# Optimization experiments

Hardware: AMD Instinct MI355X
Metric: run time of the kernel (lower is better)

Reference implementation:

```python
import jax, jax.numpy as jnp
import numpy as np
from jax import lax

K = 5        # kernel_size
KN = 32      # kernel_num
C_IN = 16
PRIOR_VAR = 0.01


def _extract_patches(x, k):
    # TF tf.image.extract_patches VALID, stride 1: last-dim order is (kh, kw, c)
    B, H, W, C = x.shape
    Ho, Wo = H - k + 1, W - k + 1
    p = jnp.stack([x[:, i:i + Ho, j:j + Wo, :] for i in range(k) for j in range(k)], axis=3)
    return p.reshape(B, Ho * Wo, k * k * C)  # [B, P, k*k*C]


def setup_inputs() -> dict:
    key = jax.random.key(0)
    k1, k2, k3, k4 = jax.random.split(key, 4)
    mu_in = jax.random.normal(k1, (32, 64, 64, C_IN), dtype=jnp.float32)
    Sigma_in = jax.random.uniform(k2, (32, 64, 64, C_IN), dtype=jnp.float32)
    # GlorotNormal for w_mu
    fan_in = K * K * C_IN
    fan_out = K * K * KN
    std = jnp.sqrt(2.0 / (fan_in + fan_out)).astype(jnp.float32)
    w_mu = jax.random.normal(k3, (K, K, C_IN, KN), dtype=jnp.float32) * std
    w_sigma = jax.random.uniform(k4, (KN,), dtype=jnp.float32, minval=-4.6, maxval=-2.25)
    return {"mu_in": mu_in, "Sigma_in": Sigma_in, "w_mu": w_mu, "w_sigma": w_sigma}


def reference(mu_in, Sigma_in, w_mu, w_sigma):
    B = mu_in.shape[0]
    # KL regularizer (broadcast w_sigma over w_mu shape, mean over all)
    kl_loss = (jnp.log(PRIOR_VAR) - 1.0 - w_sigma
               + jax.nn.softplus(w_sigma) / PRIOR_VAR
               + jnp.square(w_mu) / PRIOR_VAR)
    kl_conv = 0.5 * jnp.mean(kl_loss)

    w_sigma_2 = jax.nn.softplus(w_sigma)  # [KN]

    # mean path: standard conv
    mu_out = lax.conv_general_dilated(
        mu_in, w_mu, window_strides=(1, 1), padding='VALID',
        dimension_numbers=('NHWC', 'HWIO', 'NHWC'))  # [B, Ho, Wo, KN]
    Ho = mu_out.shape[1]

    mu_dim = jnp.float32(K * K * C_IN)

    diag_sigma_g = _extract_patches(Sigma_in, K)          # [B, P, D]
    mu_in_patches = _extract_patches(mu_in, K)            # [B, P, D]

    mu_cov_square = jnp.square(w_mu).reshape(K * K * C_IN, KN)
    mu_wT_sigmags_mu_w = diag_sigma_g @ (mu_cov_square / mu_dim)          # [B, P, KN]
    trace = jnp.sum(diag_sigma_g, axis=2, keepdims=True) * w_sigma_2 / mu_dim  # [B, P, KN]
    mu_gT_mu_g = jnp.sum(jnp.square(mu_in_patches), axis=-1, keepdims=True)    # [B, P, 1]
    sigmaw_mu_gT_mu_g = mu_gT_mu_g * w_sigma_2 / mu_dim                   # [B, P, KN]

    Sigma_out = trace + mu_wT_sigmags_mu_w + sigmaw_mu_gT_mu_g
    Sigma_out = jax.nn.softplus(Sigma_out.reshape(B, Ho, Ho, KN))
    return mu_out, Sigma_out, kl_conv
```

## Files before the change

kernel.cpp:

```cpp
#include <hip/hip_runtime.h>
#include <hip/hip_bf16.h>
#include <math.h>

#define KK 5
#define KN 32
#define CIN 16
#define H 64
#define W 64
#define NB 32
#define HO 60
#define WO 60
#define D_TOT 400
#define OUT_PLANE (NB*HO*WO*KN)

#define TH 8
#define TW 16
#define IN_R 12
#define IN_C 20
#define CPAD 24
#define TILE_SH (IN_R*IN_C*CPAD)
#define NKSTEP 13

typedef short short8 __attribute__((ext_vector_type(8)));
typedef float f32x4 __attribute__((ext_vector_type(4)));

__device__ __forceinline__ ushort f2bf(float x) {
    __hip_bfloat16 h = __float2bfloat16(x);
    return *reinterpret_cast<ushort*>(&h);
}
__device__ __forceinline__ float bf2f(ushort u) {
    __hip_bfloat16 h = *reinterpret_cast<__hip_bfloat16*>(&u);
    return __bfloat162float(h);
}
__device__ __forceinline__ ushort4 pk4(float4 v) {
    union { __hip_bfloat162 h; ushort2 u; } a, b;
    a.h = __float22bfloat162_rn(make_float2(v.x, v.y));
    b.h = __float22bfloat162_rn(make_float2(v.z, v.w));
    ushort4 r;
    r.x = a.u.x; r.y = a.u.y; r.z = b.u.x; r.w = b.u.y;
    return r;
}
__device__ __forceinline__ float softplusf(float x) {
    return (x > 20.0f) ? x : __logf(1.0f + __expf(x));
}

__global__ void prep_all(const float* __restrict__ w_mu, const float* __restrict__ w_sigma,
                         ushort* __restrict__ bmu, ushort* __restrict__ bsq,
                         float* __restrict__ spw, float* __restrict__ kl_out) {
    __shared__ float red[256];
    int t = threadIdx.x;
    if (blockIdx.x < 52) {
        int idx = blockIdx.x * 256 + t;
        int j  = idx & 7;
        int l  = (idx >> 3) & 63;
        int nt = (idx >> 9) & 1;
        int ts = idx >> 10;
        int k  = ts * 32 + ((l >> 4) & 3) * 8 + j;
        int n  = nt * 16 + (l & 15);
        if (k < D_TOT) {
            float w  = w_mu[k * KN + n];
            float sp = log1pf(expf(w_sigma[n]));
            bmu[idx] = f2bf(w);
            bsq[idx] = f2bf((w * w + sp) * (1.0f / 400.0f));
        } else {
            bmu[idx] = 0;
            bsq[idx] = 0;
        }
    } else {
        float s = 0.f;
        for (int i = t; i < D_TOT * KN; i += 256) { float w = w_mu[i]; s += w * w; }
        red[t] = s;
        __syncthreads();
        for (int off = 128; off > 0; off >>= 1) {
            if (t < off) red[t] += red[t + off];
            __syncthreads();
        }
        float sum_w2 = red[0];
        if (t < KN) {
            float ws = w_sigma[t];
            spw[t] = log1pf(expf(ws)) * (1.0f / 400.0f);
        }
        if (t == 0) {
            float sws = 0.f;
            for (int kn = 0; kn < KN; ++kn) {
                float ws = w_sigma[kn];
                float sp = log1pf(expf(ws));
                sws += -ws + sp * 100.0f;
            }
            float kl = 0.5f * (-4.605170186f - 1.0f + sws * (1.0f / 32.0f)
                               + sum_w2 * (100.0f / 12800.0f));
            *kl_out = kl;
        }
    }
}

__global__ __launch_bounds__(256, 4)
void vdp_main(const float* __restrict__ mu_in, const float* __restrict__ sig_in,
              const ushort* __restrict__ bmu_g, const ushort* __restrict__ bsq_g,
              const float* __restrict__ spw,
              float* __restrict__ mu_out, float* __restrict__ sig_out) {
    __shared__ ushort tiles[2 * TILE_SH + 8];
    __shared__ float csum[IN_R * IN_C];
    __shared__ float t12s[TH * TW];

    const int b   = blockIdx.z;
    const int ho0 = blockIdx.y * TH;
    const int wo0 = blockIdx.x * TW;
    const int t   = threadIdx.x;

    if (t < 8) tiles[2 * TILE_SH + t] = 0;

    for (int i = t; i < IN_R * IN_C * 4; i += 256) {
        int row = i / 80;
        int rem = i - row * 80;
        int col = rem >> 2, c4 = rem & 3;
        int gh = ho0 + row, gw = wo0 + col;
        float4 vm = make_float4(0.f, 0.f, 0.f, 0.f), vs = vm;
        if (gh < H && gw < W) {
            size_t g = (((size_t)b * H + gh) * W + gw) * CIN + c4 * 4;
            vm = *(const float4*)(mu_in + g);
            vs = *(const float4*)(sig_in + g);
        }
        int sb = (row * IN_C + col) * CPAD + c4 * 4;
        *(ushort4*)&tiles[sb] = pk4(vm);
        *(ushort4*)&tiles[TILE_SH + sb] = pk4(vs);
    }
    __syncthreads();

    if (t < IN_R * IN_C) {
        int sb = t * CPAD;
        float acc = 0.f;
#pragma unroll
        for (int g = 0; g < 4; ++g) {
            ushort4 m4 = *(ushort4*)&tiles[sb + g * 4];
            float m0 = bf2f(m4.x), m1 = bf2f(m4.y), m2 = bf2f(m4.z), m3 = bf2f(m4.w);
            acc += m0 * m0 + m1 * m1 + m2 * m2 + m3 * m3;
        }
        csum[t] = acc;
    }
    __syncthreads();

    if (t < TH * TW) {
        int r = t >> 4, c = t & 15;
        float s = 0.f;
#pragma unroll
        for (int kh = 0; kh < KK; ++kh)
#pragma unroll
            for (int kw = 0; kw < KK; ++kw)
                s += csum[(r + kh) * IN_C + c + kw];
        t12s[t] = s;
    }
    __syncthreads();

    const int w    = t >> 6;
    const int l    = t & 63;
    const int col  = l & 15;
    const int q    = l >> 4;
    const int qh   = q >> 1;
    const int qc   = q & 1;

    const char* lds = (const char*)tiles;
    int base0 = ((2 * w + 0) * IN_C + col) * (CPAD * 2) + qc * 16;
    int base1 = ((2 * w + 1) * IN_C + col) * (CPAD * 2) + qc * 16;
    const int qh48  = qh * 48;
    const int qh768 = qh * 768;
    const int zpad  = 2 * TILE_SH * 2;
    const int SGOFF = TILE_SH * 2;

    const short8* Bmu8 = (const short8*)bmu_g;
    const short8* Bsq8 = (const short8*)bsq_g;

    f32x4 accm[2][2], accs[2][2];
    f32x4 z = {0.f, 0.f, 0.f, 0.f};
#pragma unroll
    for (int a = 0; a < 2; ++a)
#pragma unroll
        for (int bn = 0; bn < 2; ++bn) { accm[a][bn] = z; accs[a][bn] = z; }

    constexpr int F0v[NKSTEP] = {0, 2, 4, 21, 23, 40, 42, 44, 61, 63, 80, 82, 84};
    constexpr int D16[NKSTEP] = {0, 0, 1, 0, 0, 0, 0, 1, 0, 0, 0, 0, 2};

#pragma unroll
    for (int ts = 0; ts < NKSTEP; ++ts) {
        short8 am0, am1, as0, as1;
        if (D16[ts] == 2) {
            int a0 = qh ? zpad : (base0 + F0v[ts] * 48);
            int a1 = qh ? zpad : (base1 + F0v[ts] * 48);
            am0 = *(const short8*)(lds + a0);
            am1 = *(const short8*)(lds + a1);
            as0 = *(const short8*)(lds + a0 + (qh ? 0 : SGOFF));
            as1 = *(const short8*)(lds + a1 + (qh ? 0 : SGOFF));
        } else {
            int ex = (D16[ts] ? qh768 : qh48) + F0v[ts] * 48;
            am0 = *(const short8*)(lds + base0 + ex);
            am1 = *(const short8*)(lds + base1 + ex);
            as0 = *(const short8*)(lds + SGOFF + base0 + ex);
            as1 = *(const short8*)(lds + SGOFF + base1 + ex);
        }
        short8 bm0 = Bmu8[(ts * 2 + 0) * 64 + l];
        short8 bm1 = Bmu8[(ts * 2 + 1) * 64 + l];
        short8 bs0 = Bsq8[(ts * 2 + 0) * 64 + l];
        short8 bs1 = Bsq8[(ts * 2 + 1) * 64 + l];

        accm[0][0] = __builtin_amdgcn_mfma_f32_16x16x32_bf16(am0, bm0, accm[0][0], 0, 0, 0);
        accm[0][1] = __builtin_amdgcn_mfma_f32_16x16x32_bf16(am0, bm1, accm[0][1], 0, 0, 0);
        accm[1][0] = __builtin_amdgcn_mfma_f32_16x16x32_bf16(am1, bm0, accm[1][0], 0, 0, 0);
        accm[1][1] = __builtin_amdgcn_mfma_f32_16x16x32_bf16(am1, bm1, accm[1][1], 0, 0, 0);
        accs[0][0] = __builtin_amdgcn_mfma_f32_16x16x32_bf16(as0, bs0, accs[0][0], 0, 0, 0);
        accs[0][1] = __builtin_amdgcn_mfma_f32_16x16x32_bf16(as0, bs1, accs[0][1], 0, 0, 0);
        accs[1][0] = __builtin_amdgcn_mfma_f32_16x16x32_bf16(as1, bs0, accs[1][0], 0, 0, 0);
        accs[1][1] = __builtin_amdgcn_mfma_f32_16x16x32_bf16(as1, bs1, accs[1][1], 0, 0, 0);
    }

    const float spw0 = spw[col], spw1 = spw[16 + col];
#pragma unroll
    for (int mt = 0; mt < 2; ++mt) {
        int ho = ho0 + 2 * w + mt;
        if (ho >= HO) continue;
#pragma unroll
        for (int reg = 0; reg < 4; ++reg) {
            int wo = wo0 + q * 4 + reg;
            if (wo >= WO) continue;
            float t12v = t12s[(2 * w + mt) * TW + q * 4 + reg];
            size_t basep = (((size_t)b * HO + ho) * WO + wo) * KN;
            mu_out[basep + col]      = accm[mt][0][reg];
            mu_out[basep + 16 + col] = accm[mt][1][reg];
            float s0 = accs[mt][0][reg] + t12v * spw0;
            float s1 = accs[mt][1][reg] + t12v * spw1;
            sig_out[basep + col]      = softplusf(s0);
            sig_out[basep + 16 + col] = softplusf(s1);
        }
    }
}

extern "C" void kernel_launch(void* const* d_in, const int* in_sizes, int n_in,
                              void* d_out, int out_size, void* d_ws, size_t ws_size,
                              hipStream_t stream) {
    const float* mu_in   = (const float*)d_in[0];
    const float* sig_in  = (const float*)d_in[1];
    const float* w_mu    = (const float*)d_in[2];
    const float* w_sigma = (const float*)d_in[3];

    float* out     = (float*)d_out;
    float* mu_out  = out;
    float* sig_out = out + (size_t)OUT_PLANE;
    float* kl_out  = out + 2 * (size_t)OUT_PLANE;

    ushort* bmu = (ushort*)d_ws;
    ushort* bsq = bmu + 13312;
    float*  spw = (float*)(bsq + 13312);

    prep_all<<<53, 256, 0, stream>>>(w_mu, w_sigma, bmu, bsq, spw, kl_out);
    vdp_main<<<dim3(4, 8, NB), 256, 0, stream>>>(mu_in, sig_in, bmu, bsq, spw,
                                                 mu_out, sig_out);
}
```

Before: 113.0 us.

## Process two batch images per block with register-prefetched double-buffered tiles

Each block now handles two batch images instead of one, halving the grid. The second image's input tile is loaded into registers while the first tile is processed, then written to a second LDS buffer. This aims to hide global load latency behind MFMA work. In exchange it doubles LDS use, lowers the occupancy hint from 4 to 3 blocks, and leaves fewer blocks to fill the GPU.

```diff
diff --git a/kernel.cpp b/kernel.cpp
--- a/kernel.cpp
+++ b/kernel.cpp
@@ -19,7 +19,9 @@
 #define IN_C 20
 #define CPAD 24
 #define TILE_SH (IN_R*IN_C*CPAD)
+#define BUF_BYTES (2*TILE_SH*2)
 #define NKSTEP 13
+#define NLOAD (IN_R*IN_C*4)
 
 typedef short short8 __attribute__((ext_vector_type(8)));
 typedef float f32x4 __attribute__((ext_vector_type(4)));
@@ -94,45 +96,46 @@
     }
 }
 
-__global__ __launch_bounds__(256, 4)
-void vdp_main(const float* __restrict__ mu_in, const float* __restrict__ sig_in,
-              const ushort* __restrict__ bmu_g, const ushort* __restrict__ bsq_g,
-              const float* __restrict__ spw,
-              float* __restrict__ mu_out, float* __restrict__ sig_out) {
-    __shared__ ushort tiles[2 * TILE_SH + 8];
-    __shared__ float csum[IN_R * IN_C];
-    __shared__ float t12s[TH * TW];
-
-    const int b   = blockIdx.z;
-    const int ho0 = blockIdx.y * TH;
-    const int wo0 = blockIdx.x * TW;
-    const int t   = threadIdx.x;
-
-    if (t < 8) tiles[2 * TILE_SH + t] = 0;
-
-    for (int i = t; i < IN_R * IN_C * 4; i += 256) {
-        int row = i / 80;
-        int rem = i - row * 80;
-        int col = rem >> 2, c4 = rem & 3;
-        int gh = ho0 + row, gw = wo0 + col;
-        float4 vm = make_float4(0.f, 0.f, 0.f, 0.f), vs = vm;
-        if (gh < H && gw < W) {
-            size_t g = (((size_t)b * H + gh) * W + gw) * CIN + c4 * 4;
-            vm = *(const float4*)(mu_in + g);
-            vs = *(const float4*)(sig_in + g);
-        }
-        int sb = (row * IN_C + col) * CPAD + c4 * 4;
-        *(ushort4*)&tiles[sb] = pk4(vm);
-        *(ushort4*)&tiles[TILE_SH + sb] = pk4(vs);
-    }
-    __syncthreads();
+__device__ __forceinline__ void stage_load(const float* __restrict__ mu_in,
+                                           const float* __restrict__ sig_in,
+                                           int b, int ho0, int wo0, int i,
+                                           float4& vm, float4& vs) {
+    int row = i / 80;
+    int rem = i - row * 80;
+    int col = rem >> 2, c4 = rem & 3;
+    int gh = ho0 + row, gw = wo0 + col;
+    vm = make_float4(0.f, 0.f, 0.f, 0.f); vs = vm;
+    if (gh < H && gw < W) {
+        size_t g = (((size_t)b * H + gh) * W + gw) * CIN + c4 * 4;
+        vm = *(const float4*)(mu_in + g);
+        vs = *(const float4*)(sig_in + g);
+    }
+}
+__device__ __forceinline__ void stage_write(ushort* __restrict__ buf, int i,
+                                            float4 vm, float4 vs) {
+    int row = i / 80;
+    int rem = i - row * 80;
+    int col = rem >> 2, c4 = rem & 3;
+    int sb = (row * IN_C + col) * CPAD + c4 * 4;
+    *(ushort4*)&buf[sb] = pk4(vm);
+    *(ushort4*)&buf[TILE_SH + sb] = pk4(vs);
+}
+
+__device__ __forceinline__ void process_tile(
+        const ushort* __restrict__ bufp, int zpad_rel,
+        float* __restrict__ csum, float* __restrict__ t12s,
+        const short8* __restrict__ Bmu8, const short8* __restrict__ Bsq8,
+        const float* __restrict__ spw,
+        int b, int ho0, int wo0,
+        float* __restrict__ mu_out, float* __restrict__ sig_out) {
+    const int t = threadIdx.x;
 
     if (t < IN_R * IN_C) {
         int sb = t * CPAD;
         float acc = 0.f;
 #pragma unroll
         for (int g = 0; g < 4; ++g) {
-            ushort4 m4 = *(ushort4*)&tiles[sb + g * 4];
+            ushort4 m4 = *(const ushort4*)&bufp[sb + g * 4];
             float m0 = bf2f(m4.x), m1 = bf2f(m4.y), m2 = bf2f(m4.z), m3 = bf2f(m4.w);
             acc += m0 * m0 + m1 * m1 + m2 * m2 + m3 * m3;
         }
@@ -152,30 +155,26 @@
     }
     __syncthreads();
 
-    const int w    = t >> 6;
-    const int l    = t & 63;
-    const int col  = l & 15;
-    const int q    = l >> 4;
-    const int qh   = q >> 1;
-    const int qc   = q & 1;
-
-    const char* lds = (const char*)tiles;
+    const int w   = t >> 6;
+    const int l   = t & 63;
+    const int col = l & 15;
+    const int q   = l >> 4;
+    const int qh  = q >> 1;
+    const int qc  = q & 1;
+
+    const char* lds = (const char*)bufp;
     int base0 = ((2 * w + 0) * IN_C + col) * (CPAD * 2) + qc * 16;
     int base1 = ((2 * w + 1) * IN_C + col) * (CPAD * 2) + qc * 16;
     const int qh48  = qh * 48;
     const int qh768 = qh * 768;
-    const int zpad  = 2 * TILE_SH * 2;
     const int SGOFF = TILE_SH * 2;
 
-    const short8* Bmu8 = (const short8*)bmu_g;
-    const short8* Bsq8 = (const short8*)bsq_g;
-
     f32x4 accm[2][2], accs[2][2];
-    f32x4 z = {0.f, 0.f, 0.f, 0.f};
+    f32x4 z4 = {0.f, 0.f, 0.f, 0.f};
 #pragma unroll
     for (int a = 0; a < 2; ++a)
 #pragma unroll
-        for (int bn = 0; bn < 2; ++bn) { accm[a][bn] = z; accs[a][bn] = z; }
+        for (int bn = 0; bn < 2; ++bn) { accm[a][bn] = z4; accs[a][bn] = z4; }
 
     constexpr int F0v[NKSTEP] = {0, 2, 4, 21, 23, 40, 42, 44, 61, 63, 80, 82, 84};
     constexpr int D16[NKSTEP] = {0, 0, 1, 0, 0, 0, 0, 1, 0, 0, 0, 0, 2};
@@ -184,8 +183,8 @@
     for (int ts = 0; ts < NKSTEP; ++ts) {
         short8 am0, am1, as0, as1;
         if (D16[ts] == 2) {
-            int a0 = qh ? zpad : (base0 + F0v[ts] * 48);
-            int a1 = qh ? zpad : (base1 + F0v[ts] * 48);
+            int a0 = qh ? zpad_rel : (base0 + F0v[ts] * 48);
+            int a1 = qh ? zpad_rel : (base1 + F0v[ts] * 48);
             am0 = *(const short8*)(lds + a0);
             am1 = *(const short8*)(lds + a1);
             as0 = *(const short8*)(lds + a0 + (qh ? 0 : SGOFF));
@@ -233,6 +232,55 @@
     }
 }
 
+__global__ __launch_bounds__(256, 3)
+void vdp_main(const float* __restrict__ mu_in, const float* __restrict__ sig_in,
+              const ushort* __restrict__ bmu_g, const ushort* __restrict__ bsq_g,
+              const float* __restrict__ spw,
+              float* __restrict__ mu_out, float* __restrict__ sig_out) {
+    __shared__ ushort tiles[2 * 2 * TILE_SH + 8];
+    __shared__ float csum[IN_R * IN_C];
+    __shared__ float t12s[TH * TW];
+
+    const int b0  = blockIdx.z;
+    const int b1  = blockIdx.z + 16;
+    const int ho0 = blockIdx.y * TH;
+    const int wo0 = blockIdx.x * TW;
+    const int t   = threadIdx.x;
+
+    if (t < 8) tiles[2 * 2 * TILE_SH + t] = 0;
+
+    for (int i = t; i < NLOAD; i += 256) {
+        float4 vm, vs;
+        stage_load(mu_in, sig_in, b0, ho0, wo0, i, vm, vs);
+        stage_write(tiles, i, vm, vs);
+    }
+    __syncthreads();
+
+    float4 pm[4], ps[4];
+#pragma unroll
+    for (int it = 0; it < 4; ++it) {
+        int i = t + 256 * it;
+        if (i < NLOAD) stage_load(mu_in, sig_in, b1, ho0, wo0, i, pm[it], ps[it]);
+    }
+
+    const short8* Bmu8 = (const short8*)bmu_g;
+    const short8* Bsq8 = (const short8*)bsq_g;
+
+    process_tile(tiles, 2 * BUF_BYTES, csum, t12s, Bmu8, Bsq8, spw,
+                 b0, ho0, wo0, mu_out, sig_out);
+
+    ushort* buf1 = tiles + 2 * TILE_SH;
+#pragma unroll
+    for (int it = 0; it < 4; ++it) {
+        int i = t + 256 * it;
+        if (i < NLOAD) stage_write(buf1, i, pm[it], ps[it]);
+    }
+    __syncthreads();
+
+    process_tile(buf1, BUF_BYTES, csum, t12s, Bmu8, Bsq8, spw,
+                 b1, ho0, wo0, mu_out, sig_out);
+}
+
 extern "C" void kernel_launch(void* const* d_in, const int* in_sizes, int n_in,
                               void* d_out, int out_size, void* d_ws, size_t ws_size,
                               hipStream_t stream) {
@@ -251,6 +299,6 @@
     float*  spw = (float*)(bsq + 13312);
 
     prep_all<<<53, 256, 0, stream>>>(w_mu, w_sigma, bmu, bsq, spw, kl_out);
-    vdp_main<<<dim3(4, 8, NB), 256, 0, stream>>>(mu_in, sig_in, bmu, bsq, spw,
+    vdp_main<<<dim3(4, 8, 16), 256, 0, stream>>>(mu_in, sig_in, bmu, bsq, spw,
                                                  mu_out, sig_out);
 }
```

Result: slower. 122.7 us (+8.6%).
